# Optimization experiments

Hardware: AMD Instinct MI355X
Metric: run time of the kernel (lower is better)

## Reference

```python
import jax, jax.numpy as jnp
import numpy as np

N = 100000
E = 1600000
IN_DIM, HID_DIM, LAT_DIM = 256, 128, 64


def glorot(key, shape):
    lim = float(np.sqrt(6.0 / (shape[0] + shape[1])))
    return jax.random.uniform(key, shape, jnp.float32, -lim, lim)


def setup_inputs() -> dict:
    key = jax.random.key(0)
    ks = jax.random.split(key, 8)
    x = jax.random.normal(ks[0], (N, IN_DIM), jnp.float32)
    edge_index = jax.random.randint(ks[1], (2, E), 0, N, jnp.int64)
    return {
        "x": x,
        "edge_index": edge_index,
        "W1": glorot(ks[2], (IN_DIM, HID_DIM)),
        "b1": jnp.zeros((HID_DIM,), jnp.float32),
        "Wmu": glorot(ks[3], (HID_DIM, LAT_DIM)),
        "bmu": jnp.zeros((LAT_DIM,), jnp.float32),
        "Wls": glorot(ks[4], (HID_DIM, LAT_DIM)),
        "bls": jnp.zeros((LAT_DIM,), jnp.float32),
    }


def gcn_conv(x, src, dst, norm, W, b, n_nodes):
    # PyG GCNConv: linear transform, then symmetric-normalized scatter-add
    h = x @ W                                   # [N, out]
    msg = h[src] * norm[:, None]                # [E+N, out] gathered messages
    out = jax.ops.segment_sum(msg, dst, num_segments=n_nodes)
    return out + b


def reference(x, edge_index, W1, b1, Wmu, bmu, Wls, bls):
    # add self-loops (GCNConv default)
    loop = jnp.arange(N, dtype=edge_index.dtype)
    src = jnp.concatenate([edge_index[0], loop])
    dst = jnp.concatenate([edge_index[1], loop])
    # symmetric degree normalization: deg computed on target nodes
    deg = jax.ops.segment_sum(jnp.ones_like(dst, jnp.float32), dst, num_segments=N)
    dinv = jnp.where(deg > 0, jax.lax.rsqrt(jnp.maximum(deg, 1.0)), 0.0)
    norm = dinv[src] * dinv[dst]                # [E+N]

    h = jax.nn.relu(gcn_conv(x, src, dst, norm, W1, b1, N))
    mu = gcn_conv(h, src, dst, norm, Wmu, bmu, N)
    logstd = gcn_conv(h, src, dst, norm, Wls, bls, N)
    return (mu, logstd)
```

## Files before the change

### kernel.cpp

```cpp
#include <hip/hip_runtime.h>

#define IN_DIM 256
#define HID    128
#define LAT    64
#define SLOTS  64
#define RANGE  200
#define MAXBKT 512

typedef __attribute__((ext_vector_type(8))) short short8;
typedef __attribute__((ext_vector_type(4))) float floatx4;
typedef __attribute__((ext_vector_type(4))) int  intx4;
typedef __attribute__((ext_vector_type(4))) uint uintx4;

static __device__ __forceinline__ ushort f2bf(float f) {
    union { float f; uint u; } v; v.f = f;
    uint u = v.u;
    uint r = (u + 0x7fffu + ((u >> 16) & 1u)) >> 16;
    return (ushort)r;
}
static __device__ __forceinline__ float bf_lo(uint v) { return __uint_as_float(v << 16); }
static __device__ __forceinline__ float bf_hi(uint v) { return __uint_as_float(v & 0xffff0000u); }

__global__ __launch_bounds__(256) void scatter_gemm1_kernel(
        const int* __restrict__ src, const int* __restrict__ dst,
        uint* __restrict__ bkt, int* __restrict__ bkt_cnt,
        int cap, int nbkt, int E, int sblocks,
        const float* __restrict__ X, const ushort* __restrict__ W1T,
        ushort* __restrict__ O, int N) {
    __shared__ __align__(16) char smem[28 * 1024];

    if ((int)blockIdx.x < sblocks) {
        int* cntL  = (int*)smem;
        int* baseL = cntL + MAXBKT;
        const int t = threadIdx.x;
        for (int b = t; b < nbkt; b += 256) cntL[b] = 0;
        __syncthreads();
        const int e0 = blockIdx.x * 2048 + t * 8;
        int s[8], d[8];
        if (e0 + 7 < E) {
            *(int4*)(s)     = *(const int4*)(src + e0);
            *(int4*)(s + 4) = *(const int4*)(src + e0 + 4);
            *(int4*)(d)     = *(const int4*)(dst + e0);
            *(int4*)(d + 4) = *(const int4*)(dst + e0 + 4);
        } else {
            #pragma unroll
            for (int k = 0; k < 8; ++k) {
                int e = e0 + k;
                s[k] = (e < E) ? src[e] : 0;
                d[k] = (e < E) ? dst[e] : -1;
            }
        }
        int r[8], off[8];
        #pragma unroll
        for (int k = 0; k < 8; ++k) {
            r[k] = (d[k] >= 0) ? (d[k] / RANGE) : -1;
            if (r[k] >= 0) off[k] = atomicAdd(&cntL[r[k]], 1);
        }
        __syncthreads();
        for (int b = t; b < nbkt; b += 256) {
            int c = cntL[b];
            baseL[b] = c ? atomicAdd(&bkt_cnt[b], c) : 0;
        }
        __syncthreads();
        #pragma unroll
        for (int k = 0; k < 8; ++k) {
            if (r[k] >= 0) {
                int p = baseL[r[k]] + off[k];
                if (p < cap)
                    bkt[(size_t)r[k] * cap + p] =
                        ((uint)s[k] << 8) | (uint)(d[k] - r[k] * RANGE);
            }
        }
        return;
    }

    ushort* As = (ushort*)smem;
    ushort* Bs = As + 64 * 32;
    ushort* Cs = Bs + 128 * 32;
    const int bid  = blockIdx.x - sblocks;
    const int tid  = threadIdx.x;
    const int wave = tid >> 6, lane = tid & 63;
    const int q = lane >> 4, ln = lane & 15;
    const int row0 = bid * 64;
    floatx4 acc[8] = {};

    for (int k0 = 0; k0 < IN_DIM; k0 += 32) {
        #pragma unroll
        for (int t = 0; t < 2; ++t) {
            int j = t * 256 + tid;
            int r = j >> 3, kc = (j & 7) * 4;
            float4 v = make_float4(0.f, 0.f, 0.f, 0.f);
            if (row0 + r < N)
                v = *(const float4*)(X + (size_t)(row0 + r) * IN_DIM + k0 + kc);
            *(ushort4*)(As + r * 32 + kc) =
                make_ushort4(f2bf(v.x), f2bf(v.y), f2bf(v.z), f2bf(v.w));
        }
        #pragma unroll
        for (int t = 0; t < 2; ++t) {
            int c = t * 256 + tid;
            int n = c >> 2, kc = (c & 3) * 8;
            *(int4*)(Bs + n * 32 + kc) = *(const int4*)(W1T + (size_t)n * IN_DIM + k0 + kc);
        }
        __syncthreads();
        short8 a = *(const short8*)(As + (wave * 16 + ln) * 32 + q * 8);
        #pragma unroll
        for (int t = 0; t < 8; ++t) {
            short8 b = *(const short8*)(Bs + (t * 16 + ln) * 32 + q * 8);
            acc[t] = __builtin_amdgcn_mfma_f32_16x16x32_bf16(a, b, acc[t], 0, 0, 0);
        }
        __syncthreads();
    }
    #pragma unroll
    for (int t = 0; t < 8; ++t)
        #pragma unroll
        for (int r = 0; r < 4; ++r)
            Cs[(wave * 16 + q * 4 + r) * 128 + t * 16 + ln] = f2bf(acc[t][r]);
    __syncthreads();
    #pragma unroll
    for (int t = 0; t < 4; ++t) {
        int j = t * 256 + tid;
        int r = j >> 4, c8 = (j & 15) * 8;
        if (row0 + r < N)
            *(int4*)(O + (size_t)(row0 + r) * HID + c8) = *(const int4*)(Cs + r * 128 + c8);
    }
}

__global__ __launch_bounds__(256) void fill_bin_kernel(const uint* __restrict__ bkt,
                                                       const int* __restrict__ bkt_cnt,
                                                       int* __restrict__ cur,
                                                       float* __restrict__ dinv,
                                                       int* __restrict__ csr,
                                                       int cap, int N) {
    __shared__ int lcnt[RANGE];
    __shared__ int lslots[RANGE * SLOTS];
    const int r  = blockIdx.x;
    const int lo = r * RANGE;
    const int R  = min(RANGE, N - lo);
    if (R <= 0) return;
    for (int j = threadIdx.x; j < R; j += 256) lcnt[j] = 0;
    __syncthreads();
    const int sz = min(bkt_cnt[r], cap);
    const uint* b = bkt + (size_t)r * cap;
    for (int i = threadIdx.x * 4; i + 3 < sz; i += 1024) {
        uintx4 e4 = __builtin_nontemporal_load((const uintx4*)(b + i));
        #pragma unroll
        for (int k = 0; k < 4; ++k) {
            uint e = e4[k];
            int ln = (int)(e & 255u);
            int p = atomicAdd(&lcnt[ln], 1);
            if (p < SLOTS) lslots[(ln << 6) + p] = (int)(e >> 8);
        }
    }
    {
        int k = (sz & ~3) + threadIdx.x;
        if (k < sz) {
            uint e = b[k];
            int ln = (int)(e & 255u);
            int p = atomicAdd(&lcnt[ln], 1);
            if (p < SLOTS) lslots[(ln << 6) + p] = (int)(e >> 8);
        }
    }
    __syncthreads();
    const int nInt4 = R << 4;
    int4* dstp = (int4*)(csr + ((size_t)lo << 6));
    const int4* srcp = (const int4*)lslots;
    for (int j = threadIdx.x; j < nInt4; j += 256)
        dstp[j] = srcp[j];
    for (int j = threadIdx.x; j < R; j += 256) {
        int c = lcnt[j];
        cur[lo + j]  = c;
        dinv[lo + j] = rsqrtf((float)(c + 1));
    }
}

__global__ void prep_weights(const float* __restrict__ W1, const float* __restrict__ Wmu,
                             const float* __restrict__ Wls,
                             ushort* __restrict__ W1T, ushort* __restrict__ W2T,
                             int* __restrict__ bkt_cnt) {
    int idx = blockIdx.x * 256 + threadIdx.x;
    if (idx < MAXBKT) bkt_cnt[idx] = 0;
    if (idx < IN_DIM * HID) {
        int n = idx & 127, k = idx >> 7;
        W1T[n * IN_DIM + k] = f2bf(W1[idx]);
    } else {
        int j = idx - IN_DIM * HID;
        if (j < HID * LAT) {
            int n = j & 63, k = j >> 6;
            W2T[n * HID + k] = f2bf(Wmu[j]);
        } else {
            int jj = j - HID * LAT;
            int n = jj & 63, k = jj >> 6;
            W2T[(64 + n) * HID + k] = f2bf(Wls[jj]);
        }
    }
}

#define EDGE4(JB)                                                        \
    {                                                                    \
        int   s_ = __shfl(e,  (JB));                                     \
        float n_ = __shfl(nr, (JB));                                     \
        uint4 v_ = *(const uint4*)(inb + (size_t)s_ * HID);              \
        a0 += bf_lo(v_.x) * n_; a1 += bf_hi(v_.x) * n_;                  \
        a2 += bf_lo(v_.y) * n_; a3 += bf_hi(v_.y) * n_;                  \
        a4 += bf_lo(v_.z) * n_; a5 += bf_hi(v_.z) * n_;                  \
        a6 += bf_lo(v_.w) * n_; a7 += bf_hi(v_.w) * n_;                  \
    }

__global__ __launch_bounds__(256) void agg_kernel(const ushort* __restrict__ in,
                                                  ushort* __restrict__ out,
                                                  const int* __restrict__ cnt,
                                                  const int* __restrict__ csr,
                                                  const float* __restrict__ dinv,
                                                  const float* __restrict__ bias,
                                                  int N, int mode) {
    int wid  = (blockIdx.x * 256 + threadIdx.x) >> 6;
    int lane = threadIdx.x & 63;
    if (wid >= N) return;
    const int cn   = min(cnt[wid], SLOTS);
    const float dd = dinv[wid];
    int e    = (cn > 0) ? csr[(wid << 6) + min(lane, cn - 1)] : wid;
    float nr = dinv[e] * dd;
    const int q    = lane >> 4;
    const int boff = (lane & 15) * 8;
    const ushort* inb = in + boff;
    float a0=0.f,a1=0.f,a2=0.f,a3=0.f,a4=0.f,a5=0.f,a6=0.f,a7=0.f;
    const int nfull = cn >> 2;
    int jj = 0;
    for (; jj + 4 <= nfull; jj += 4) {
        int j0 = (jj << 2) + q;
        EDGE4(j0); EDGE4(j0 + 4); EDGE4(j0 + 8); EDGE4(j0 + 12);
    }
    for (; jj + 2 <= nfull; jj += 2) {
        int j0 = (jj << 2) + q;
        EDGE4(j0); EDGE4(j0 + 4);
    }
    if (jj < nfull) {
        EDGE4((jj << 2) + q);
    }
    {
        int rem = cn - (nfull << 2);
        int jT  = max(min((nfull << 2) + q, cn - 1), 0);
        int   sT = __shfl(e,  jT);
        float nT = __shfl(nr, jT);
        if (q < rem) {
            uint4 v0 = *(const uint4*)(inb + (size_t)sT * HID);
            a0 += bf_lo(v0.x) * nT; a1 += bf_hi(v0.x) * nT;
            a2 += bf_lo(v0.y) * nT; a3 += bf_hi(v0.y) * nT;
            a4 += bf_lo(v0.z) * nT; a5 += bf_hi(v0.z) * nT;
            a6 += bf_lo(v0.w) * nT; a7 += bf_hi(v0.w) * nT;
        }
    }
    a0 += __shfl_xor(a0, 16); a1 += __shfl_xor(a1, 16);
    a2 += __shfl_xor(a2, 16); a3 += __shfl_xor(a3, 16);
    a4 += __shfl_xor(a4, 16); a5 += __shfl_xor(a5, 16);
    a6 += __shfl_xor(a6, 16); a7 += __shfl_xor(a7, 16);
    a0 += __shfl_xor(a0, 32); a1 += __shfl_xor(a1, 32);
    a2 += __shfl_xor(a2, 32); a3 += __shfl_xor(a3, 32);
    a4 += __shfl_xor(a4, 32); a5 += __shfl_xor(a5, 32);
    a6 += __shfl_xor(a6, 32); a7 += __shfl_xor(a7, 32);
    if (q == 0) {
        {
            uint4 sv = *(const uint4*)(in + (size_t)wid * HID + boff);
            float ss = dd * dd;
            a0 += bf_lo(sv.x) * ss; a1 += bf_hi(sv.x) * ss;
            a2 += bf_lo(sv.y) * ss; a3 += bf_hi(sv.y) * ss;
            a4 += bf_lo(sv.z) * ss; a5 += bf_hi(sv.z) * ss;
            a6 += bf_lo(sv.w) * ss; a7 += bf_hi(sv.w) * ss;
        }
        if (mode) {
            float4 b0 = *(const float4*)(bias + boff);
            float4 b1 = *(const float4*)(bias + boff + 4);
            a0 = fmaxf(a0 + b0.x, 0.f); a1 = fmaxf(a1 + b0.y, 0.f);
            a2 = fmaxf(a2 + b0.z, 0.f); a3 = fmaxf(a3 + b0.w, 0.f);
            a4 = fmaxf(a4 + b1.x, 0.f); a5 = fmaxf(a5 + b1.y, 0.f);
            a6 = fmaxf(a6 + b1.z, 0.f); a7 = fmaxf(a7 + b1.w, 0.f);
        }
        uint4 pk;
        pk.x = (uint)f2bf(a0) | ((uint)f2bf(a1) << 16);
        pk.y = (uint)f2bf(a2) | ((uint)f2bf(a3) << 16);
        pk.z = (uint)f2bf(a4) | ((uint)f2bf(a5) << 16);
        pk.w = (uint)f2bf(a6) | ((uint)f2bf(a7) << 16);
        *(uint4*)(out + (size_t)wid * HID + boff) = pk;
    }
}

__global__ __launch_bounds__(256) void gemm2_mfma(const ushort* __restrict__ G,
                                                  const ushort* __restrict__ W2T,
                                                  const float* __restrict__ bmu,
                                                  const float* __restrict__ bls,
                                                  float* __restrict__ mu,
                                                  float* __restrict__ ls, int N) {
    __shared__ ushort As[64 * 32];
    __shared__ ushort Bs[128 * 32];
    __shared__ float  Cs[64 * 128];
    const int tid  = threadIdx.x;
    const int wave = tid >> 6, lane = tid & 63;
    const int q = lane >> 4, ln = lane & 15;
    const int row0 = blockIdx.x * 64;
    floatx4 acc[8] = {};

    for (int k0 = 0; k0 < HID; k0 += 32) {
        {
            int r = tid >> 2, kc = (tid & 3) * 8;
            int4 v = make_int4(0, 0, 0, 0);
            if (row0 + r < N) v = *(const int4*)(G + (size_t)(row0 + r) * HID + k0 + kc);
            *(int4*)(As + r * 32 + kc) = v;
        }
        #pragma unroll
        for (int t = 0; t < 2; ++t) {
            int c = t * 256 + tid;
            int n = c >> 2, kc = (c & 3) * 8;
            *(int4*)(Bs + n * 32 + kc) = *(const int4*)(W2T + (size_t)n * HID + k0 + kc);
        }
        __syncthreads();
        short8 a = *(const short8*)(As + (wave * 16 + ln) * 32 + q * 8);
        #pragma unroll
        for (int t = 0; t < 8; ++t) {
            short8 b = *(const short8*)(Bs + (t * 16 + ln) * 32 + q * 8);
            acc[t] = __builtin_amdgcn_mfma_f32_16x16x32_bf16(a, b, acc[t], 0, 0, 0);
        }
        __syncthreads();
    }
    #pragma unroll
    for (int t = 0; t < 8; ++t)
        #pragma unroll
        for (int r = 0; r < 4; ++r)
            Cs[(wave * 16 + q * 4 + r) * 128 + t * 16 + ln] = acc[t][r];
    __syncthreads();
    #pragma unroll
    for (int t = 0; t < 8; ++t) {
        int j = t * 256 + tid;
        int r = j >> 5, c4 = (j & 31) * 4;
        if (row0 + r < N) {
            float4 v = *(const float4*)(Cs + r * 128 + c4);
            if (c4 < 64) {
                float4 b = *(const float4*)(bmu + c4);
                *(float4*)(mu + (size_t)(row0 + r) * LAT + c4) =
                    make_float4(v.x + b.x, v.y + b.y, v.z + b.z, v.w + b.w);
            } else {
                float4 b = *(const float4*)(bls + (c4 - 64));
                *(float4*)(ls + (size_t)(row0 + r) * LAT + (c4 - 64)) =
                    make_float4(v.x + b.x, v.y + b.y, v.z + b.z, v.w + b.w);
            }
        }
    }
}

extern "C" void kernel_launch(void* const* d_in, const int* in_sizes, int n_in,
                              void* d_out, int out_size, void* d_ws, size_t ws_size,
                              hipStream_t stream) {
    const float* x    = (const float*)d_in[0];
    const int*   edge = (const int*)d_in[1];
    const float* W1   = (const float*)d_in[2];
    const float* b1   = (const float*)d_in[3];
    const float* Wmu  = (const float*)d_in[4];
    const float* bmu  = (const float*)d_in[5];
    const float* Wls  = (const float*)d_in[6];
    const float* bls  = (const float*)d_in[7];

    const int N    = in_sizes[0] / IN_DIM;
    const int E    = in_sizes[1] / 2;
    const int nbkt = (N + RANGE - 1) / RANGE;
    const int cap  = 4096;

    const int* src = edge;
    const int* dst = edge + E;

    ushort* t1b  = (ushort*)d_ws;
    ushort* hb   = t1b + (size_t)N * HID;
    int*    csr  = (int*)(hb + (size_t)N * HID);
    uint*   bkt  = (uint*)(csr + (size_t)N * SLOTS);
    float*  dinv = (float*)(bkt + (size_t)MAXBKT * cap);
    int*    cur  = (int*)(dinv + N);
    int* bkt_cnt = cur + N;
    ushort* W1T  = (ushort*)(bkt_cnt + MAXBKT);
    ushort* W2T  = W1T + IN_DIM * HID;
    ushort* gb   = t1b;

    float* mu = (float*)d_out;
    float* ls = mu + (size_t)N * LAT;

    prep_weights<<<(IN_DIM * HID + 2 * HID * LAT) / 256, 256, 0, stream>>>(
        W1, Wmu, Wls, W1T, W2T, bkt_cnt);

    {
        int sblocks  = (E + 2047) / 2048;
        int g1blocks = (N + 63) / 64;
        scatter_gemm1_kernel<<<sblocks + g1blocks, 256, 0, stream>>>(
            src, dst, bkt, bkt_cnt, cap, nbkt, E, sblocks, x, W1T, t1b, N);
    }

    fill_bin_kernel<<<nbkt, 256, 0, stream>>>(bkt, bkt_cnt, cur, dinv, csr, cap, N);

    {
        int blocks = (int)(((long long)N * 64 + 255) / 256);
        agg_kernel<<<blocks, 256, 0, stream>>>(t1b, hb, cur, csr, dinv, b1, N, 1);
    }
    {
        int blocks = (int)(((long long)N * 64 + 255) / 256);
        agg_kernel<<<blocks, 256, 0, stream>>>(hb, gb, cur, csr, dinv, nullptr, N, 0);
    }

    gemm2_mfma<<<(N + 63) / 64, 256, 0, stream>>>(gb, W2T, bmu, bls, mu, ls, N);
}
```

Measured before the change: 374.1 us.

## Fuse CSR fill, both aggregations and second GEMM into one cooperative kernel

Replaces the fill_bin, two agg and gemm2 launches with a single persistent cooperative kernel that uses grid-wide syncs between phases, removing launch gaps and tail effects. It also halves the bucket range so more blocks share the fill work, sizes the bucket capacity from the edge count, and writes the GEMM output straight from registers instead of staging it through LDS. The trade-offs are grid.sync overhead, lower occupancy from the fixed persistent grid, and stores to mu and ls that are less well coalesced.

```diff
diff --git a/kernel.cpp b/kernel.cpp
--- a/kernel.cpp
+++ b/kernel.cpp
@@ -1,15 +1,16 @@
 #include <hip/hip_runtime.h>
+#include <hip/hip_cooperative_groups.h>
+namespace cg = cooperative_groups;
 
 #define IN_DIM 256
 #define HID    128
 #define LAT    64
 #define SLOTS  64
-#define RANGE  200
-#define MAXBKT 512
+#define RANGE  100
+#define MAXBKT 1024
 
 typedef __attribute__((ext_vector_type(8))) short short8;
 typedef __attribute__((ext_vector_type(4))) float floatx4;
-typedef __attribute__((ext_vector_type(4))) int  intx4;
 typedef __attribute__((ext_vector_type(4))) uint uintx4;
 
 static __device__ __forceinline__ ushort f2bf(float f) {
@@ -125,54 +126,6 @@
     }
 }
 
-__global__ __launch_bounds__(256) void fill_bin_kernel(const uint* __restrict__ bkt,
-                                                       const int* __restrict__ bkt_cnt,
-                                                       int* __restrict__ cur,
-                                                       float* __restrict__ dinv,
-                                                       int* __restrict__ csr,
-                                                       int cap, int N) {
-    __shared__ int lcnt[RANGE];
-    __shared__ int lslots[RANGE * SLOTS];
-    const int r  = blockIdx.x;
-    const int lo = r * RANGE;
-    const int R  = min(RANGE, N - lo);
-    if (R <= 0) return;
-    for (int j = threadIdx.x; j < R; j += 256) lcnt[j] = 0;
-    __syncthreads();
-    const int sz = min(bkt_cnt[r], cap);
-    const uint* b = bkt + (size_t)r * cap;
-    for (int i = threadIdx.x * 4; i + 3 < sz; i += 1024) {
-        uintx4 e4 = __builtin_nontemporal_load((const uintx4*)(b + i));
-        #pragma unroll
-        for (int k = 0; k < 4; ++k) {
-            uint e = e4[k];
-            int ln = (int)(e & 255u);
-            int p = atomicAdd(&lcnt[ln], 1);
-            if (p < SLOTS) lslots[(ln << 6) + p] = (int)(e >> 8);
-        }
-    }
-    {
-        int k = (sz & ~3) + threadIdx.x;
-        if (k < sz) {
-            uint e = b[k];
-            int ln = (int)(e & 255u);
-            int p = atomicAdd(&lcnt[ln], 1);
-            if (p < SLOTS) lslots[(ln << 6) + p] = (int)(e >> 8);
-        }
-    }
-    __syncthreads();
-    const int nInt4 = R << 4;
-    int4* dstp = (int4*)(csr + ((size_t)lo << 6));
-    const int4* srcp = (const int4*)lslots;
-    for (int j = threadIdx.x; j < nInt4; j += 256)
-        dstp[j] = srcp[j];
-    for (int j = threadIdx.x; j < R; j += 256) {
-        int c = lcnt[j];
-        cur[lo + j]  = c;
-        dinv[lo + j] = rsqrtf((float)(c + 1));
-    }
-}
-
 __global__ void prep_weights(const float* __restrict__ W1, const float* __restrict__ Wmu,
                              const float* __restrict__ Wls,
                              ushort* __restrict__ W1T, ushort* __restrict__ W2T,
@@ -206,16 +159,14 @@
         a6 += bf_lo(v_.w) * n_; a7 += bf_hi(v_.w) * n_;                  \
     }
 
-__global__ __launch_bounds__(256) void agg_kernel(const ushort* __restrict__ in,
-                                                  ushort* __restrict__ out,
-                                                  const int* __restrict__ cnt,
-                                                  const int* __restrict__ csr,
-                                                  const float* __restrict__ dinv,
-                                                  const float* __restrict__ bias,
-                                                  int N, int mode) {
-    int wid  = (blockIdx.x * 256 + threadIdx.x) >> 6;
-    int lane = threadIdx.x & 63;
-    if (wid >= N) return;
+template<int MODE>
+static __device__ __forceinline__ void agg_node(const ushort* __restrict__ in,
+                                                ushort* __restrict__ out,
+                                                const int* __restrict__ cnt,
+                                                const int* __restrict__ csr,
+                                                const float* __restrict__ dinv,
+                                                const float* __restrict__ bias,
+                                                int wid, int lane) {
     const int cn   = min(cnt[wid], SLOTS);
     const float dd = dinv[wid];
     int e    = (cn > 0) ? csr[(wid << 6) + min(lane, cn - 1)] : wid;
@@ -267,7 +218,7 @@
             a4 += bf_lo(sv.z) * ss; a5 += bf_hi(sv.z) * ss;
             a6 += bf_lo(sv.w) * ss; a7 += bf_hi(sv.w) * ss;
         }
-        if (mode) {
+        if (MODE) {
             float4 b0 = *(const float4*)(bias + boff);
             float4 b1 = *(const float4*)(bias + boff + 4);
             a0 = fmaxf(a0 + b0.x, 0.f); a1 = fmaxf(a1 + b0.y, 0.f);
@@ -284,63 +235,115 @@
     }
 }
 
-__global__ __launch_bounds__(256) void gemm2_mfma(const ushort* __restrict__ G,
-                                                  const ushort* __restrict__ W2T,
-                                                  const float* __restrict__ bmu,
-                                                  const float* __restrict__ bls,
-                                                  float* __restrict__ mu,
-                                                  float* __restrict__ ls, int N) {
-    __shared__ ushort As[64 * 32];
-    __shared__ ushort Bs[128 * 32];
-    __shared__ float  Cs[64 * 128];
-    const int tid  = threadIdx.x;
-    const int wave = tid >> 6, lane = tid & 63;
-    const int q = lane >> 4, ln = lane & 15;
-    const int row0 = blockIdx.x * 64;
-    floatx4 acc[8] = {};
-
-    for (int k0 = 0; k0 < HID; k0 += 32) {
-        {
-            int r = tid >> 2, kc = (tid & 3) * 8;
-            int4 v = make_int4(0, 0, 0, 0);
-            if (row0 + r < N) v = *(const int4*)(G + (size_t)(row0 + r) * HID + k0 + kc);
-            *(int4*)(As + r * 32 + kc) = v;
-        }
-        #pragma unroll
-        for (int t = 0; t < 2; ++t) {
-            int c = t * 256 + tid;
-            int n = c >> 2, kc = (c & 3) * 8;
-            *(int4*)(Bs + n * 32 + kc) = *(const int4*)(W2T + (size_t)n * HID + k0 + kc);
-        }
-        __syncthreads();
-        short8 a = *(const short8*)(As + (wave * 16 + ln) * 32 + q * 8);
-        #pragma unroll
-        for (int t = 0; t < 8; ++t) {
-            short8 b = *(const short8*)(Bs + (t * 16 + ln) * 32 + q * 8);
-            acc[t] = __builtin_amdgcn_mfma_f32_16x16x32_bf16(a, b, acc[t], 0, 0, 0);
-        }
-        __syncthreads();
-    }
-    #pragma unroll
-    for (int t = 0; t < 8; ++t)
-        #pragma unroll
-        for (int r = 0; r < 4; ++r)
-            Cs[(wave * 16 + q * 4 + r) * 128 + t * 16 + ln] = acc[t][r];
-    __syncthreads();
-    #pragma unroll
-    for (int t = 0; t < 8; ++t) {
-        int j = t * 256 + tid;
-        int r = j >> 5, c4 = (j & 31) * 4;
-        if (row0 + r < N) {
-            float4 v = *(const float4*)(Cs + r * 128 + c4);
-            if (c4 < 64) {
-                float4 b = *(const float4*)(bmu + c4);
-                *(float4*)(mu + (size_t)(row0 + r) * LAT + c4) =
-                    make_float4(v.x + b.x, v.y + b.y, v.z + b.z, v.w + b.w);
-            } else {
-                float4 b = *(const float4*)(bls + (c4 - 64));
-                *(float4*)(ls + (size_t)(row0 + r) * LAT + (c4 - 64)) =
-                    make_float4(v.x + b.x, v.y + b.y, v.z + b.z, v.w + b.w);
+__global__ __launch_bounds__(256, 6) void tail_coop_kernel(
+        const uint* __restrict__ bkt, const int* __restrict__ bkt_cnt,
+        int* __restrict__ cur, float* __restrict__ dinv, int* __restrict__ csr,
+        int cap, int N, int nbkt,
+        const ushort* __restrict__ t1b, ushort* __restrict__ hb, ushort* __restrict__ gb,
+        const float* __restrict__ b1, const ushort* __restrict__ W2T,
+        const float* __restrict__ bmu, const float* __restrict__ bls,
+        float* __restrict__ mu, float* __restrict__ ls) {
+    cg::grid_group grid = cg::this_grid();
+    __shared__ __align__(16) char smem[26 * 1024];
+    const int wave = threadIdx.x >> 6, lane = threadIdx.x & 63;
+
+    {
+        int* lcnt   = (int*)smem;
+        int* lslots = lcnt + RANGE;
+        for (int r = blockIdx.x; r < nbkt; r += gridDim.x) {
+            const int lo = r * RANGE;
+            const int R  = min(RANGE, N - lo);
+            if (R <= 0) break;
+            for (int j = threadIdx.x; j < R; j += 256) lcnt[j] = 0;
+            __syncthreads();
+            const int sz = min(bkt_cnt[r], cap);
+            const uint* b = bkt + (size_t)r * cap;
+            for (int i = threadIdx.x * 4; i + 3 < sz; i += 1024) {
+                uintx4 e4 = __builtin_nontemporal_load((const uintx4*)(b + i));
+                #pragma unroll
+                for (int k = 0; k < 4; ++k) {
+                    uint e = e4[k];
+                    int ln = (int)(e & 255u);
+                    int p = atomicAdd(&lcnt[ln], 1);
+                    if (p < SLOTS) lslots[(ln << 6) + p] = (int)(e >> 8);
+                }
+            }
+            {
+                int k = (sz & ~3) + threadIdx.x;
+                if (k < sz) {
+                    uint e = b[k];
+                    int ln = (int)(e & 255u);
+                    int p = atomicAdd(&lcnt[ln], 1);
+                    if (p < SLOTS) lslots[(ln << 6) + p] = (int)(e >> 8);
+                }
+            }
+            __syncthreads();
+            const int nInt4 = R << 4;
+            int4* dstp = (int4*)(csr + ((size_t)lo << 6));
+            const int4* srcp = (const int4*)lslots;
+            for (int j = threadIdx.x; j < nInt4; j += 256)
+                dstp[j] = srcp[j];
+            for (int j = threadIdx.x; j < R; j += 256) {
+                int c = lcnt[j];
+                cur[lo + j]  = c;
+                dinv[lo + j] = rsqrtf((float)(c + 1));
+            }
+            __syncthreads();
+        }
+    }
+    grid.sync();
+
+    for (int wid = blockIdx.x * 4 + wave; wid < N; wid += gridDim.x * 4)
+        agg_node<1>(t1b, hb, cur, csr, dinv, b1, wid, lane);
+    grid.sync();
+
+    for (int wid = blockIdx.x * 4 + wave; wid < N; wid += gridDim.x * 4)
+        agg_node<0>(hb, gb, cur, csr, dinv, nullptr, wid, lane);
+    grid.sync();
+
+    {
+        ushort* As = (ushort*)smem;
+        ushort* Bs = As + 64 * 32;
+        const int tid = threadIdx.x;
+        const int q = lane >> 4, ln = lane & 15;
+        for (int bid = blockIdx.x; bid * 64 < N; bid += gridDim.x) {
+            const int row0 = bid * 64;
+            floatx4 acc[8] = {};
+            for (int k0 = 0; k0 < HID; k0 += 32) {
+                {
+                    int r = tid >> 2, kc = (tid & 3) * 8;
+                    int4 v = make_int4(0, 0, 0, 0);
+                    if (row0 + r < N) v = *(const int4*)(gb + (size_t)(row0 + r) * HID + k0 + kc);
+                    *(int4*)(As + r * 32 + kc) = v;
+                }
+                #pragma unroll
+                for (int t = 0; t < 2; ++t) {
+                    int c = t * 256 + tid;
+                    int n = c >> 2, kc = (c & 3) * 8;
+                    *(int4*)(Bs + n * 32 + kc) = *(const int4*)(W2T + (size_t)n * HID + k0 + kc);
+                }
+                __syncthreads();
+                short8 a = *(const short8*)(As + (wave * 16 + ln) * 32 + q * 8);
+                #pragma unroll
+                for (int t = 0; t < 8; ++t) {
+                    short8 b = *(const short8*)(Bs + (t * 16 + ln) * 32 + q * 8);
+                    acc[t] = __builtin_amdgcn_mfma_f32_16x16x32_bf16(a, b, acc[t], 0, 0, 0);
+                }
+                __syncthreads();
+            }
+            #pragma unroll
+            for (int t = 0; t < 8; ++t) {
+                int col = t * 16 + ln;
+                float bv = (col < 64) ? bmu[col] : bls[col - 64];
+                #pragma unroll
+                for (int r = 0; r < 4; ++r) {
+                    int row = row0 + wave * 16 + q * 4 + r;
+                    if (row < N) {
+                        float v = acc[t][r] + bv;
+                        if (col < 64) mu[(size_t)row * LAT + col] = v;
+                        else          ls[(size_t)row * LAT + (col - 64)] = v;
+                    }
+                }
             }
         }
     }
@@ -361,7 +364,8 @@
     const int N    = in_sizes[0] / IN_DIM;
     const int E    = in_sizes[1] / 2;
     const int nbkt = (N + RANGE - 1) / RANGE;
-    const int cap  = 4096;
+    int cap = E / nbkt + 512;
+    cap = (cap + 3) & ~3;
 
     const int* src = edge;
     const int* dst = edge + E;
@@ -380,6 +384,23 @@
     float* mu = (float*)d_out;
     float* ls = mu + (size_t)N * LAT;
 
+    static int coopBlocks = 0;
+    if (coopBlocks == 0) {
+        int mab = 0;
+        if (hipOccupancyMaxActiveBlocksPerMultiprocessor(&mab, tail_coop_kernel, 256, 0)
+                != hipSuccess || mab <= 0)
+            mab = 4;
+        int cus = 256;
+        hipDeviceProp_t prop;
+        int dev = 0;
+        if (hipGetDevice(&dev) == hipSuccess &&
+            hipGetDeviceProperties(&prop, dev) == hipSuccess)
+            cus = prop.multiProcessorCount;
+        coopBlocks = mab * cus;
+        if (coopBlocks < 256) coopBlocks = 256;
+        if (coopBlocks > 4096) coopBlocks = 4096;
+    }
+
     prep_weights<<<(IN_DIM * HID + 2 * HID * LAT) / 256, 256, 0, stream>>>(
         W1, Wmu, Wls, W1T, W2T, bkt_cnt);
 
@@ -390,16 +411,14 @@
             src, dst, bkt, bkt_cnt, cap, nbkt, E, sblocks, x, W1T, t1b, N);
     }
 
-    fill_bin_kernel<<<nbkt, 256, 0, stream>>>(bkt, bkt_cnt, cur, dinv, csr, cap, N);
-
     {
-        int blocks = (int)(((long long)N * 64 + 255) / 256);
-        agg_kernel<<<blocks, 256, 0, stream>>>(t1b, hb, cur, csr, dinv, b1, N, 1);
-    }
-    {
-        int blocks = (int)(((long long)N * 64 + 255) / 256);
-        agg_kernel<<<blocks, 256, 0, stream>>>(hb, gb, cur, csr, dinv, nullptr, N, 0);
-    }
-
-    gemm2_mfma<<<(N + 63) / 64, 256, 0, stream>>>(gb, W2T, bmu, bls, mu, ls, N);
-}
+        void* args[] = { (void*)&bkt, (void*)&bkt_cnt, (void*)&cur, (void*)&dinv,
+                         (void*)&csr, (void*)&cap, (void*)&N, (void*)&nbkt,
+                         (void*)&t1b, (void*)&hb, (void*)&gb,
+                         (void*)&b1, (void*)&W2T, (void*)&bmu, (void*)&bls,
+                         (void*)&mu, (void*)&ls };
+        (void)hipLaunchCooperativeKernel((const void*)tail_coop_kernel,
+                                         dim3(coopBlocks), dim3(256),
+                                         args, 0, stream);
+    }
+}
```

Result: slower. 708.2 us (+89.3%).
